# Kernel tuning notes

Measured on AMD Instinct MI355X. Metric: run time of the kernel, lower is better.

## Reference

```python
import jax, jax.numpy as jnp
import numpy as np

HEADS = 16
DIM_HEAD = 64
DIM = 1024
INNER = HEADS * DIM_HEAD


def setup_inputs() -> dict:
    key = jax.random.key(0)
    k1, k2, k3, k4 = jax.random.split(key, 4)
    x = jax.random.normal(k1, (4, 2048, DIM), dtype=jnp.float32)
    W_qkv = jax.random.normal(k2, (DIM, 3 * INNER), dtype=jnp.float32) * (DIM ** -0.5)
    W_out = jax.random.normal(k3, (INNER, DIM), dtype=jnp.float32) * (INNER ** -0.5)
    b_out = jax.random.normal(k4, (DIM,), dtype=jnp.float32) * 0.01
    temperature = jnp.asarray(np.log(DIM_HEAD ** -0.5), dtype=jnp.float32)
    return {"x": x, "W_qkv": W_qkv, "W_out": W_out, "b_out": b_out,
            "temperature": temperature}


def reference(x, W_qkv, W_out, b_out, temperature):
    b, n, _ = x.shape
    qkv = jnp.einsum('bnd,de->bne', x, W_qkv)  # [b, n, 3*inner]
    q, k, v = jnp.split(qkv, 3, axis=-1)
    def split_heads(t):
        return t.reshape(b, n, HEADS, DIM_HEAD).transpose(0, 2, 1, 3)  # b h n d
    q, k, v = split_heads(q), split_heads(k), split_heads(v)
    scale = jnp.exp(temperature)
    dots = jnp.einsum('bhid,bhjd->bhij', q, k) * scale  # [b, h, n, n]
    mask_value = -jnp.finfo(dots.dtype).max
    eye = jnp.eye(n, dtype=bool)
    dots = jnp.where(eye, mask_value, dots)
    attn = jax.nn.softmax(dots, axis=-1)
    out = jnp.einsum('bhij,bhjd->bhid', attn, v)  # [b, h, n, d]
    out = out.transpose(0, 2, 1, 3).reshape(b, n, INNER)
    return jnp.einsum('bni,id->bnd', out, W_out) + b_out
```

## Files before the change

### kernel.cpp

```cpp
#include <hip/hip_runtime.h>


using u16 = unsigned short;
typedef short short8 __attribute__((ext_vector_type(8)));
typedef float floatx4 __attribute__((ext_vector_type(4)));
typedef float floatx16 __attribute__((ext_vector_type(16)));
typedef unsigned int uint2v __attribute__((ext_vector_type(2)));

#define B_ 4
#define N_ 2048
#define H_ 16
#define DH_ 64
#define D_ 1024
#define INNER_ 1024
#define M_ (B_ * N_)

__device__ __forceinline__ float bf2f(u16 h) {
    union { unsigned u; float f; } c; c.u = ((unsigned)h) << 16; return c.f;
}
__device__ __forceinline__ u16 f2bf(float f) {
    union { float f; unsigned u; } c; c.f = f;
    unsigned u = c.u + 0x7fffu + ((c.u >> 16) & 1u);
    return (u16)(u >> 16);
}
__device__ __forceinline__ unsigned cvtpk_bf16(float lo, float hi) {
    unsigned r;
    asm("v_cvt_pk_bf16_f32 %0, %1, %2" : "=v"(r) : "v"(lo), "v"(hi));
    return r;
}
__device__ __forceinline__ float fast_exp2(float x) {
#if defined(__has_builtin) && __has_builtin(__builtin_amdgcn_exp2f)
    return __builtin_amdgcn_exp2f(x);
#else
    return __expf(x * 0.69314718056f);
#endif
}
__device__ __forceinline__ void gl2lds16(const u16* g, u16* l) {
    __builtin_amdgcn_global_load_lds(
        (const __attribute__((address_space(1))) void*)g,
        (__attribute__((address_space(3))) void*)l, 16, 0, 0);
}

__global__ void detect_prep(const u16* __restrict__ x, int* __restrict__ flag,
                            const void* __restrict__ bias_in,
                            const void* __restrict__ temp_in,
                            float* __restrict__ bias_f,
                            float* __restrict__ temp_f) {
    __shared__ int cnt;
    __shared__ int fl;
    if (threadIdx.x == 0) cnt = 0;
    __syncthreads();
    int c = 0;
    for (int i = threadIdx.x; i < 4096; i += 256) {
        int e = (x[i] >> 7) & 0xFF;
        if (e >= 107 && e <= 147) c++;
    }
    atomicAdd(&cnt, c);
    __syncthreads();
    if (threadIdx.x == 0) { fl = (cnt >= 3584) ? 1 : 0; flag[0] = fl; }
    __syncthreads();
    const int f = fl;
    for (int i = threadIdx.x; i < 1024; i += 256)
        bias_f[i] = f ? bf2f(((const u16*)bias_in)[i]) : ((const float*)bias_in)[i];
    if (threadIdx.x == 0)
        temp_f[0] = f ? bf2f(((const u16*)temp_in)[0]) : ((const float*)temp_in)[0];
}

__global__ __launch_bounds__(256) void prep_inputs(
    const void* __restrict__ x, u16* __restrict__ xb,
    const void* __restrict__ Wqkv, u16* __restrict__ Wqkv_t,
    const void* __restrict__ Wout, u16* __restrict__ Wout_t,
    const int* __restrict__ flag) {
    __shared__ u16 t[32][33];
    const int f = flag[0];
    const int b = blockIdx.x;
    if (b < 4096) {
        long i0 = ((long)b * 256 + threadIdx.x) * 8;
        u16 tmp[8];
        if (f) {
            *(short8*)tmp = *(const short8*)((const u16*)x + i0);
        } else {
            const float* p = (const float*)x + i0;
            for (int i = 0; i < 8; i++) tmp[i] = f2bf(p[i]);
        }
        *(short8*)&xb[i0] = *(const short8*)tmp;
        return;
    }
    const void* in;
    u16* out;
    int bx, by, R, C;
    if (b < 4096 + 3072) {
        int idx = b - 4096;
        bx = idx % 96; by = idx / 96; R = D_; C = 3 * INNER_;
        in = Wqkv; out = Wqkv_t;
    } else {
        int idx = b - 7168;
        bx = idx % 32; by = idx / 32; R = INNER_; C = D_;
        in = Wout; out = Wout_t;
    }
    int tx = threadIdx.x & 31, ty = threadIdx.x >> 5;
    int c0 = bx * 32, r0 = by * 32;
    for (int i = 0; i < 4; i++) {
        long idx = (long)(r0 + ty + i * 8) * C + c0 + tx;
        t[ty + i * 8][tx] = f ? ((const u16*)in)[idx] : f2bf(((const float*)in)[idx]);
    }
    __syncthreads();
    for (int i = 0; i < 4; i++)
        out[(long)(c0 + ty + i * 8) * R + r0 + tx] = t[tx][ty + i * 8];
}

__global__ __launch_bounds__(256) void transpose_v(
    const u16* __restrict__ in, u16* __restrict__ out) {
    __shared__ u16 t[32][33];
    const int bh = blockIdx.z;
    const u16* src = in + (long)bh * N_ * DH_;
    u16* dst = out + (long)bh * DH_ * N_;
    int tx = threadIdx.x & 31, ty = threadIdx.x >> 5;
    int r0 = blockIdx.y * 32;
    int c0 = blockIdx.x * 32;
    for (int i = 0; i < 4; i++)
        t[ty + i * 8][tx] = src[(long)(r0 + ty + i * 8) * DH_ + c0 + tx];
    __syncthreads();
    for (int i = 0; i < 4; i++)
        dst[(long)(c0 + ty + i * 8) * N_ + r0 + tx] = t[tx][ty + i * 8];
}

template <int MODE>
__global__ __launch_bounds__(256) void gemm_bt(
    const u16* __restrict__ A, const u16* __restrict__ Bt,
    int M, int N, int K,
    u16* __restrict__ out0, u16* __restrict__ out1, u16* __restrict__ out2,
    void* __restrict__ outv, const float* __restrict__ bias,
    const int* __restrict__ flag, const float* __restrict__ temp_f) {
    __shared__ __align__(16) u16 lA[128 * 32];
    __shared__ __align__(16) u16 lB[128 * 32];
    const int tid = threadIdx.x;
    const int lane = tid & 63;
    const int w = tid >> 6;
    const int wr = w >> 1, wc = w & 1;
    const int qd = lane >> 4, qm = lane & 15;
    const long m0 = (long)blockIdx.x * 128;
    const long n0 = (long)blockIdx.y * 128;

    floatx4 acc[4][4];
    for (int i = 0; i < 4; i++)
        for (int j = 0; j < 4; j++) acc[i][j] = (floatx4){0.f, 0.f, 0.f, 0.f};

    const int arow = lane >> 2;
    const int acol = ((lane & 3) ^ ((lane >> 3) & 3)) * 8;
    const int swz = (qm >> 1) & 3;

    for (int k0 = 0; k0 < K; k0 += 32) {
        for (int i = 0; i < 2; i++) {
            int c = w + i * 4;
            gl2lds16(A + (m0 + c * 16 + arow) * K + k0 + acol, lA + c * 512);
            gl2lds16(Bt + (n0 + c * 16 + arow) * K + k0 + acol, lB + c * 512);
        }
        __syncthreads();
        short8 af[4], bfr[4];
        for (int mt = 0; mt < 4; mt++)
            af[mt] = *(const short8*)&lA[(wr * 64 + mt * 16 + qm) * 32 + (qd ^ swz) * 8];
        for (int nt = 0; nt < 4; nt++)
            bfr[nt] = *(const short8*)&lB[(wc * 64 + nt * 16 + qm) * 32 + (qd ^ swz) * 8];
        for (int mt = 0; mt < 4; mt++)
            for (int nt = 0; nt < 4; nt++)
                acc[mt][nt] = __builtin_amdgcn_mfma_f32_16x16x32_bf16(
                    af[mt], bfr[nt], acc[mt][nt], 0, 0, 0);
        __syncthreads();
    }

    if (MODE == 0) {
        const float qscale = __expf(temp_f[0]) * 1.44269504089f;
        __shared__ __align__(16) u16 lC[64 * 132];
        for (int half = 0; half < 2; half++) {
            __syncthreads();
            if (wr == half) {
                for (int nt = 0; nt < 4; nt++) {
                    long ng = n0 + wc * 64 + nt * 16 + qm;
                    float sc = ((ng >> 10) == 0) ? qscale : 1.0f;
                    for (int mt = 0; mt < 4; mt++)
                        for (int r = 0; r < 4; r++)
                            lC[(mt * 16 + qd * 4 + r) * 132 + wc * 64 + nt * 16 + qm] =
                                f2bf(acc[mt][nt][r] * sc);
                }
            }
            __syncthreads();
            for (int i = 0; i < 4; i++) {
                int row = (tid >> 4) + i * 16;
                int c = (tid & 15) * 8;
                long m = m0 + half * 64 + row;
                long ngc = n0 + c;
                int part = (int)(ngc >> 10);
                int rem = (int)(ngc & 1023);
                int hh = rem >> 6, dh = rem & 63;
                long bb = m >> 11, n = m & 2047;
                long idx = ((bb * H_ + hh) * N_ + n) * DH_ + dh;
                short8 vv = *(const short8*)&lC[row * 132 + c];
                u16* dst = (part == 0) ? out0 : (part == 1) ? out1 : out2;
                *(short8*)&dst[idx] = vv;
            }
        }
    } else {
        const int f = flag[0];
        __shared__ __align__(16) float lCf[64 * 132];
        for (int half = 0; half < 2; half++) {
            __syncthreads();
            if (wr == half) {
                for (int nt = 0; nt < 4; nt++) {
                    long ng = n0 + wc * 64 + nt * 16 + qm;
                    float bv = bias[ng];
                    for (int mt = 0; mt < 4; mt++)
                        for (int r = 0; r < 4; r++)
                            lCf[(mt * 16 + qd * 4 + r) * 132 + wc * 64 + nt * 16 + qm] =
                                acc[mt][nt][r] + bv;
                }
            }
            __syncthreads();
            if (f) {
                for (int i = 0; i < 4; i++) {
                    int row = (tid >> 4) + i * 16;
                    int c = (tid & 15) * 8;
                    long m = m0 + half * 64 + row;
                    u16 tmp[8];
                    for (int j = 0; j < 8; j++) tmp[j] = f2bf(lCf[row * 132 + c + j]);
                    __builtin_nontemporal_store(*(const short8*)tmp,
                        (short8*)&((u16*)outv)[m * N + n0 + c]);
                }
            } else {
                for (int i = 0; i < 8; i++) {
                    int row = (tid >> 5) + i * 8;
                    int c = (tid & 31) * 4;
                    long m = m0 + half * 64 + row;
                    floatx4 vv = *(const floatx4*)&lCf[row * 132 + c];
                    __builtin_nontemporal_store(vv,
                        (floatx4*)&((float*)outv)[m * N + n0 + c]);
                }
            }
        }
    }
}

__global__ __launch_bounds__(256) void attn_full(
    const u16* __restrict__ q_ws, const u16* __restrict__ k_ws,
    const u16* __restrict__ vt_ws, u16* __restrict__ out) {
    __shared__ __align__(16) u16 lbuf[2 * 2 * 64 * 64];
    const int tid = threadIdx.x, lane = tid & 63, w = tid >> 6;
    const int ln = lane & 31, h = lane >> 5;

    int linear = blockIdx.y * 8 + blockIdx.x;
    int bh = (linear & 7) * 8 + ((linear >> 6) & 7);
    int q0 = ((linear >> 3) & 7) * 256;
    const int b = bh >> 4, hd = bh & 15;

    const u16* Q = q_ws + (long)bh * N_ * DH_;
    const u16* Kp = k_ws + (long)bh * N_ * DH_;
    const u16* Vt = vt_ws + (long)bh * DH_ * N_;

    const int qbase = q0 + w * 64;

    short8 qa[2][4];
#pragma unroll
    for (int g = 0; g < 2; g++)
#pragma unroll
        for (int c = 0; c < 4; c++)
            qa[g][c] = *(const short8*)
                &Q[(long)(qbase + g * 32 + ln) * DH_ + c * 16 + h * 8];

    floatx16 accO[2][2];
#pragma unroll
    for (int i = 0; i < 16; i++) {
        accO[0][0][i] = 0.f; accO[0][1][i] = 0.f;
        accO[1][0][i] = 0.f; accO[1][1][i] = 0.f;
    }
    float lacc[2] = {0.f, 0.f};

    const int srow = lane >> 3;
    const int scol = ((lane & 7) ^ srow) * 8;
    const int rsw = (ln & 7);

    {
        u16* nK = lbuf;
        u16* nV = lbuf + 4096;
        for (int i = 0; i < 2; i++) {
            int c = w + i * 4;
            gl2lds16(Kp + (long)(c * 8 + srow) * DH_ + scol, nK + c * 512);
            gl2lds16(Vt + (long)(c * 8 + srow) * N_ + scol, nV + c * 512);
        }
    }
    __syncthreads();

    for (int t = 0; t < 32; t++) {
        const int k0 = t * 64;
        const u16* lK = lbuf + (t & 1) * 8192;
        const u16* lV = lK + 4096;
        if (t < 31) {
            u16* nK = lbuf + ((t + 1) & 1) * 8192;
            u16* nV = nK + 4096;
            for (int i = 0; i < 2; i++) {
                int c = w + i * 4;
                gl2lds16(Kp + (long)(k0 + 64 + c * 8 + srow) * DH_ + scol,
                         nK + c * 512);
                gl2lds16(Vt + (long)(c * 8 + srow) * N_ + k0 + 64 + scol,
                         nV + c * 512);
            }
        }

#pragma unroll
        for (int kt = 0; kt < 2; kt++) {
            floatx16 accS[2];
#pragma unroll
            for (int i = 0; i < 16; i++) { accS[0][i] = 0.f; accS[1][i] = 0.f; }
#pragma unroll
            for (int c = 0; c < 4; c++) {
                short8 kf = *(const short8*)
                    &lK[(kt * 32 + ln) * 64 + ((c * 2 + h) ^ rsw) * 8];
                accS[0] = __builtin_amdgcn_mfma_f32_32x32x16_bf16(
                    kf, qa[0][c], accS[0], 0, 0, 0);
                accS[1] = __builtin_amdgcn_mfma_f32_32x32x16_bf16(
                    kf, qa[1][c], accS[1], 0, 0, 0);
            }
#pragma unroll
            for (int g = 0; g < 2; g++) {
#pragma unroll
                for (int r = 0; r < 16; r++)
                    accS[g][r] = fast_exp2(accS[g][r]);
                if ((qbase + g * 32) == (k0 + kt * 32)) {
#pragma unroll
                    for (int r = 0; r < 16; r++) {
                        int kk = (r & 3) + 8 * (r >> 2) + 4 * h;
                        if (kk == ln) accS[g][r] = 0.f;
                    }
                }
                float rs = (((accS[g][0] + accS[g][1]) + (accS[g][2] + accS[g][3]))
                          + ((accS[g][4] + accS[g][5]) + (accS[g][6] + accS[g][7])))
                         + (((accS[g][8] + accS[g][9]) + (accS[g][10] + accS[g][11]))
                          + ((accS[g][12] + accS[g][13]) + (accS[g][14] + accS[g][15])));
                lacc[g] += rs;
            }
#pragma unroll
            for (int ch = 0; ch < 2; ch++) {
                const int rb = ch * 8;
                short8 pfv[2];
#pragma unroll
                for (int g = 0; g < 2; g++) {
                    unsigned d01 = cvtpk_bf16(accS[g][rb + 0], accS[g][rb + 1]);
                    unsigned d23 = cvtpk_bf16(accS[g][rb + 2], accS[g][rb + 3]);
                    unsigned d45 = cvtpk_bf16(accS[g][rb + 4], accS[g][rb + 5]);
                    unsigned d67 = cvtpk_bf16(accS[g][rb + 6], accS[g][rb + 7]);
                    uint2v s1 = __builtin_amdgcn_permlane32_swap(d01, d45, false, false);
                    uint2v s2 = __builtin_amdgcn_permlane32_swap(d23, d67, false, false);
                    union { unsigned u[4]; short8 v; } pf;
                    pf.u[0] = s1[0]; pf.u[1] = s2[0]; pf.u[2] = s1[1]; pf.u[3] = s2[1];
                    pfv[g] = pf.v;
                }
                const int cc = kt * 2 + ch;
#pragma unroll
                for (int dt = 0; dt < 2; dt++) {
                    short8 vf = *(const short8*)
                        &lV[(dt * 32 + ln) * 64 + ((cc * 2 + h) ^ rsw) * 8];
                    accO[0][dt] = __builtin_amdgcn_mfma_f32_32x32x16_bf16(
                        vf, pfv[0], accO[0][dt], 0, 0, 0);
                    accO[1][dt] = __builtin_amdgcn_mfma_f32_32x32x16_bf16(
                        vf, pfv[1], accO[1][dt], 0, 0, 0);
                }
            }
        }
        __syncthreads();
    }

#pragma unroll
    for (int g = 0; g < 2; g++) {
        float s = lacc[g];
        s += __shfl_xor(s, 32, 64);
        const float inv = 1.f / s;
        u16* stg = (u16*)((char*)lbuf + w * 8192 + g * 4096);
#pragma unroll
        for (int dt = 0; dt < 2; dt++)
#pragma unroll
            for (int q2 = 0; q2 < 4; q2++) {
                union { unsigned u[2]; unsigned long long ull; } ee;
                ee.u[0] = cvtpk_bf16(accO[g][dt][q2 * 4 + 0] * inv,
                                     accO[g][dt][q2 * 4 + 1] * inv);
                ee.u[1] = cvtpk_bf16(accO[g][dt][q2 * 4 + 2] * inv,
                                     accO[g][dt][q2 * 4 + 3] * inv);
                int G = dt * 4 + q2;
                *(unsigned long long*)
                    &stg[ln * 64 + ((G ^ rsw) * 8) + h * 4] = ee.ull;
            }
    }
    __syncthreads();
#pragma unroll
    for (int p = 0; p < 8; p++) {
        int R = p * 32 + (tid >> 3);
        int G = tid & 7;
        const u16* src = (const u16*)((char*)lbuf + (R >> 6) * 8192
                          + ((R >> 5) & 1) * 4096
                          + (R & 31) * 128 + ((G ^ (R & 7)) * 16));
        short8 vv = *(const short8*)src;
        *(short8*)&out[((long)(b * N_ + q0 + R)) * INNER_ + hd * DH_ + G * 8] = vv;
    }
}

extern "C" void kernel_launch(void* const* d_in, const int* in_sizes, int n_in,
                              void* d_out, int out_size, void* d_ws, size_t ws_size,
                              hipStream_t stream) {
    const void* x    = d_in[0];
    const void* Wqkv = d_in[1];
    const void* Wout = d_in[2];
    const void* bout = d_in[3];
    const void* temp = d_in[4];

    char* base = (char*)d_ws;
    int*   flag    = (int*)base;
    float* temp_f  = (float*)(base + 16);
    float* bias_f  = (float*)(base + 32);
    u16* xb      = (u16*)(base + 8192);
    u16* Wqkv_t  = xb + (long)M_ * D_;
    u16* Wout_t  = Wqkv_t + 3072 * 1024;
    u16* q_ws    = Wout_t + 1024 * 1024;
    u16* k_ws    = q_ws + (long)B_ * H_ * N_ * DH_;
    u16* vt_ws   = k_ws + (long)B_ * H_ * N_ * DH_;
    u16* attn_out = vt_ws + (long)B_ * H_ * N_ * DH_;
    u16* v_nat   = attn_out;

    dim3 blk(256);
    detect_prep<<<1, blk, 0, stream>>>((const u16*)x, flag, bout, temp,
                                       bias_f, temp_f);
    prep_inputs<<<dim3(4096 + 3072 + 1024), blk, 0, stream>>>(
        x, xb, Wqkv, Wqkv_t, Wout, Wout_t, flag);
    gemm_bt<0><<<dim3(M_ / 128, 3 * INNER_ / 128), blk, 0, stream>>>(
        xb, Wqkv_t, M_, 3 * INNER_, D_, q_ws, k_ws, v_nat, nullptr, nullptr,
        flag, temp_f);
    transpose_v<<<dim3(DH_ / 32, N_ / 32, B_ * H_), blk, 0, stream>>>(
        v_nat, vt_ws);
    attn_full<<<dim3(8, 64), blk, 0, stream>>>(
        q_ws, k_ws, vt_ws, attn_out);
    gemm_bt<1><<<dim3(M_ / 128, D_ / 128), blk, 0, stream>>>(
        attn_out, Wout_t, M_, D_, INNER_, nullptr, nullptr, nullptr, d_out,
        bias_f, flag, temp_f);
}
```

Measured before the change: 285.7 us.

## Double-buffer GEMM LDS tiles and alias epilogue staging onto shared buffer

Turns the GEMM k-loop into a two-stage LDS double buffer. The next tile's global-to-LDS loads are issued before the MFMAs on the current tile, which removes one barrier per iteration and overlaps memory with compute. The epilogue staging buffers now reuse the same shared allocation, which keeps total LDS near its previous size. In MODE 1 the float staging pitch drops from 132 to 128 so it fits, at the risk of LDS bank conflicts in the epilogue writes.

```diff
diff --git a/kernel.cpp b/kernel.cpp
--- a/kernel.cpp
+++ b/kernel.cpp
@@ -132,8 +132,7 @@
     u16* __restrict__ out0, u16* __restrict__ out1, u16* __restrict__ out2,
     void* __restrict__ outv, const float* __restrict__ bias,
     const int* __restrict__ flag, const float* __restrict__ temp_f) {
-    __shared__ __align__(16) u16 lA[128 * 32];
-    __shared__ __align__(16) u16 lB[128 * 32];
+    __shared__ __align__(16) u16 smem[16384];
     const int tid = threadIdx.x;
     const int lane = tid & 63;
     const int w = tid >> 6;
@@ -150,13 +149,31 @@
     const int acol = ((lane & 3) ^ ((lane >> 3) & 3)) * 8;
     const int swz = (qm >> 1) & 3;
 
-    for (int k0 = 0; k0 < K; k0 += 32) {
+    {
+        u16* lA = smem;
+        u16* lB = smem + 4096;
         for (int i = 0; i < 2; i++) {
             int c = w + i * 4;
-            gl2lds16(A + (m0 + c * 16 + arow) * K + k0 + acol, lA + c * 512);
-            gl2lds16(Bt + (n0 + c * 16 + arow) * K + k0 + acol, lB + c * 512);
-        }
-        __syncthreads();
+            gl2lds16(A + (m0 + c * 16 + arow) * K + acol, lA + c * 512);
+            gl2lds16(Bt + (n0 + c * 16 + arow) * K + acol, lB + c * 512);
+        }
+    }
+    __syncthreads();
+
+    const int nT = K >> 5;
+    for (int t = 0; t < nT; ++t) {
+        const u16* lA = smem + (t & 1) * 8192;
+        const u16* lB = lA + 4096;
+        if (t + 1 < nT) {
+            u16* nA = smem + ((t + 1) & 1) * 8192;
+            u16* nB = nA + 4096;
+            const int k1 = (t + 1) << 5;
+            for (int i = 0; i < 2; i++) {
+                int c = w + i * 4;
+                gl2lds16(A + (m0 + c * 16 + arow) * K + k1 + acol, nA + c * 512);
+                gl2lds16(Bt + (n0 + c * 16 + arow) * K + k1 + acol, nB + c * 512);
+            }
+        }
         short8 af[4], bfr[4];
         for (int mt = 0; mt < 4; mt++)
             af[mt] = *(const short8*)&lA[(wr * 64 + mt * 16 + qm) * 32 + (qd ^ swz) * 8];
@@ -171,7 +188,7 @@
 
     if (MODE == 0) {
         const float qscale = __expf(temp_f[0]) * 1.44269504089f;
-        __shared__ __align__(16) u16 lC[64 * 132];
+        u16* lC = smem;
         for (int half = 0; half < 2; half++) {
             __syncthreads();
             if (wr == half) {
@@ -202,7 +219,7 @@
         }
     } else {
         const int f = flag[0];
-        __shared__ __align__(16) float lCf[64 * 132];
+        float* lCf = (float*)smem;
         for (int half = 0; half < 2; half++) {
             __syncthreads();
             if (wr == half) {
@@ -211,7 +228,7 @@
                     float bv = bias[ng];
                     for (int mt = 0; mt < 4; mt++)
                         for (int r = 0; r < 4; r++)
-                            lCf[(mt * 16 + qd * 4 + r) * 132 + wc * 64 + nt * 16 + qm] =
+                            lCf[(mt * 16 + qd * 4 + r) * 128 + wc * 64 + nt * 16 + qm] =
                                 acc[mt][nt][r] + bv;
                 }
             }
@@ -222,7 +239,7 @@
                     int c = (tid & 15) * 8;
                     long m = m0 + half * 64 + row;
                     u16 tmp[8];
-                    for (int j = 0; j < 8; j++) tmp[j] = f2bf(lCf[row * 132 + c + j]);
+                    for (int j = 0; j < 8; j++) tmp[j] = f2bf(lCf[row * 128 + c + j]);
                     __builtin_nontemporal_store(*(const short8*)tmp,
                         (short8*)&((u16*)outv)[m * N + n0 + c]);
                 }
@@ -231,7 +248,7 @@
                     int row = (tid >> 5) + i * 8;
                     int c = (tid & 31) * 4;
                     long m = m0 + half * 64 + row;
-                    floatx4 vv = *(const floatx4*)&lCf[row * 132 + c];
+                    floatx4 vv = *(const floatx4*)&lCf[row * 128 + c];
                     __builtin_nontemporal_store(vv,
                         (floatx4*)&((float*)outv)[m * N + n0 + c]);
                 }
```

Measured after the change: 289.4 us. About the same (+1.3%).

## Double-buffer GEMM LDS loads with larger 128x256 tiles and 512 threads

Applied to the files above, without the earlier changes.

The projection GEMM kernel moves to 512-thread blocks computing 128x256 output tiles with a K-step of 64. The next K-slice is prefetched into a second LDS buffer while the current one is consumed, which removes one barrier per iteration. The swizzle changes to an 8-way XOR and the epilogue reuses the shared buffer. The aim is to hide global-load latency and raise arithmetic intensity, at the cost of 96KB of LDS per block (lower occupancy) and fewer blocks in the grid.

```diff
diff --git a/kernel.cpp b/kernel.cpp
--- a/kernel.cpp
+++ b/kernel.cpp
@@ -126,112 +126,137 @@
 }
 
 template <int MODE>
-__global__ __launch_bounds__(256) void gemm_bt(
+__global__ __launch_bounds__(512) void gemm_bt(
     const u16* __restrict__ A, const u16* __restrict__ Bt,
     int M, int N, int K,
     u16* __restrict__ out0, u16* __restrict__ out1, u16* __restrict__ out2,
     void* __restrict__ outv, const float* __restrict__ bias,
     const int* __restrict__ flag, const float* __restrict__ temp_f) {
-    __shared__ __align__(16) u16 lA[128 * 32];
-    __shared__ __align__(16) u16 lB[128 * 32];
+    __shared__ __align__(16) u16 smem[49152];
     const int tid = threadIdx.x;
     const int lane = tid & 63;
     const int w = tid >> 6;
-    const int wr = w >> 1, wc = w & 1;
+    const int wm = w >> 2, wn = w & 3;
     const int qd = lane >> 4, qm = lane & 15;
     const long m0 = (long)blockIdx.x * 128;
-    const long n0 = (long)blockIdx.y * 128;
+    const long n0 = (long)blockIdx.y * 256;
 
     floatx4 acc[4][4];
     for (int i = 0; i < 4; i++)
         for (int j = 0; j < 4; j++) acc[i][j] = (floatx4){0.f, 0.f, 0.f, 0.f};
 
-    const int arow = lane >> 2;
-    const int acol = ((lane & 3) ^ ((lane >> 3) & 3)) * 8;
-    const int swz = (qm >> 1) & 3;
-
-    for (int k0 = 0; k0 < K; k0 += 32) {
-        for (int i = 0; i < 2; i++) {
-            int c = w + i * 4;
-            gl2lds16(A + (m0 + c * 16 + arow) * K + k0 + acol, lA + c * 512);
-            gl2lds16(Bt + (n0 + c * 16 + arow) * K + k0 + acol, lB + c * 512);
-        }
-        __syncthreads();
-        short8 af[4], bfr[4];
-        for (int mt = 0; mt < 4; mt++)
-            af[mt] = *(const short8*)&lA[(wr * 64 + mt * 16 + qm) * 32 + (qd ^ swz) * 8];
-        for (int nt = 0; nt < 4; nt++)
-            bfr[nt] = *(const short8*)&lB[(wc * 64 + nt * 16 + qm) * 32 + (qd ^ swz) * 8];
-        for (int mt = 0; mt < 4; mt++)
-            for (int nt = 0; nt < 4; nt++)
-                acc[mt][nt] = __builtin_amdgcn_mfma_f32_16x16x32_bf16(
-                    af[mt], bfr[nt], acc[mt][nt], 0, 0, 0);
+    const int sr = tid >> 3;
+    const int sg = tid & 7;
+    const int scol = (sg ^ (sr & 7)) * 8;
+    const int rx = qm & 7;
+
+    for (int c = 0; c < 2; c++)
+        gl2lds16(A + (m0 + c * 64 + sr) * K + scol, smem + c * 4096 + tid * 8);
+    for (int c = 0; c < 4; c++)
+        gl2lds16(Bt + (n0 + c * 64 + sr) * K + scol,
+                 smem + 8192 + c * 4096 + tid * 8);
+    __syncthreads();
+
+    const int nT = K >> 6;
+    for (int t = 0; t < nT; ++t) {
+        const u16* lA = smem + (t & 1) * 24576;
+        const u16* lB = lA + 8192;
+        if (t + 1 < nT) {
+            u16* nb = smem + ((t + 1) & 1) * 24576;
+            const int k1 = (t + 1) << 6;
+            for (int c = 0; c < 2; c++)
+                gl2lds16(A + (m0 + c * 64 + sr) * K + k1 + scol,
+                         nb + c * 4096 + tid * 8);
+            for (int c = 0; c < 4; c++)
+                gl2lds16(Bt + (n0 + c * 64 + sr) * K + k1 + scol,
+                         nb + 8192 + c * 4096 + tid * 8);
+        }
+#pragma unroll
+        for (int s = 0; s < 2; s++) {
+            short8 af[4], bf[4];
+#pragma unroll
+            for (int mr = 0; mr < 4; mr++)
+                af[mr] = *(const short8*)
+                    &lA[(wm * 64 + mr * 16 + qm) * 64 + (((s * 4 + qd) ^ rx) * 8)];
+#pragma unroll
+            for (int nr = 0; nr < 4; nr++)
+                bf[nr] = *(const short8*)
+                    &lB[(wn * 64 + nr * 16 + qm) * 64 + (((s * 4 + qd) ^ rx) * 8)];
+#pragma unroll
+            for (int mr = 0; mr < 4; mr++)
+#pragma unroll
+                for (int nr = 0; nr < 4; nr++)
+                    acc[mr][nr] = __builtin_amdgcn_mfma_f32_16x16x32_bf16(
+                        af[mr], bf[nr], acc[mr][nr], 0, 0, 0);
+        }
         __syncthreads();
     }
 
     if (MODE == 0) {
         const float qscale = __expf(temp_f[0]) * 1.44269504089f;
-        __shared__ __align__(16) u16 lC[64 * 132];
+        const int part = (int)(n0 >> 10);
+        const float sc = (part == 0) ? qscale : 1.0f;
+        u16* lC = smem;
         for (int half = 0; half < 2; half++) {
             __syncthreads();
-            if (wr == half) {
-                for (int nt = 0; nt < 4; nt++) {
-                    long ng = n0 + wc * 64 + nt * 16 + qm;
-                    float sc = ((ng >> 10) == 0) ? qscale : 1.0f;
-                    for (int mt = 0; mt < 4; mt++)
+            if (wm == half) {
+                for (int nr = 0; nr < 4; nr++) {
+                    int col = wn * 64 + nr * 16 + qm;
+                    for (int mr = 0; mr < 4; mr++)
                         for (int r = 0; r < 4; r++)
-                            lC[(mt * 16 + qd * 4 + r) * 132 + wc * 64 + nt * 16 + qm] =
-                                f2bf(acc[mt][nt][r] * sc);
+                            lC[(mr * 16 + qd * 4 + r) * 264 + col] =
+                                f2bf(acc[mr][nr][r] * sc);
                 }
             }
             __syncthreads();
+            const long mb = m0 + half * 64;
+            const long bb = mb >> 11;
+            const int  nb = (int)(mb & 2047);
             for (int i = 0; i < 4; i++) {
-                int row = (tid >> 4) + i * 16;
-                int c = (tid & 15) * 8;
-                long m = m0 + half * 64 + row;
+                int row = (tid >> 5) + i * 16;
+                int c = (tid & 31) * 8;
                 long ngc = n0 + c;
-                int part = (int)(ngc >> 10);
+                int pt = (int)(ngc >> 10);
                 int rem = (int)(ngc & 1023);
                 int hh = rem >> 6, dh = rem & 63;
-                long bb = m >> 11, n = m & 2047;
-                long idx = ((bb * H_ + hh) * N_ + n) * DH_ + dh;
-                short8 vv = *(const short8*)&lC[row * 132 + c];
-                u16* dst = (part == 0) ? out0 : (part == 1) ? out1 : out2;
+                long idx = ((bb * H_ + hh) * N_ + (nb + row)) * DH_ + dh;
+                short8 vv = *(const short8*)&lC[row * 264 + c];
+                u16* dst = (pt == 0) ? out0 : (pt == 1) ? out1 : out2;
                 *(short8*)&dst[idx] = vv;
             }
         }
     } else {
         const int f = flag[0];
-        __shared__ __align__(16) float lCf[64 * 132];
+        float* lCf = (float*)smem;
         for (int half = 0; half < 2; half++) {
             __syncthreads();
-            if (wr == half) {
-                for (int nt = 0; nt < 4; nt++) {
-                    long ng = n0 + wc * 64 + nt * 16 + qm;
+            if (wm == half) {
+                for (int nr = 0; nr < 4; nr++) {
+                    long ng = n0 + wn * 64 + nr * 16 + qm;
                     float bv = bias[ng];
-                    for (int mt = 0; mt < 4; mt++)
+                    for (int mr = 0; mr < 4; mr++)
                         for (int r = 0; r < 4; r++)
-                            lCf[(mt * 16 + qd * 4 + r) * 132 + wc * 64 + nt * 16 + qm] =
-                                acc[mt][nt][r] + bv;
+                            lCf[(mr * 16 + qd * 4 + r) * 260 + wn * 64 + nr * 16 + qm] =
+                                acc[mr][nr][r] + bv;
                 }
             }
             __syncthreads();
             if (f) {
                 for (int i = 0; i < 4; i++) {
-                    int row = (tid >> 4) + i * 16;
-                    int c = (tid & 15) * 8;
+                    int row = (tid >> 5) + i * 16;
+                    int c = (tid & 31) * 8;
                     long m = m0 + half * 64 + row;
                     u16 tmp[8];
-                    for (int j = 0; j < 8; j++) tmp[j] = f2bf(lCf[row * 132 + c + j]);
+                    for (int j = 0; j < 8; j++) tmp[j] = f2bf(lCf[row * 260 + c + j]);
                     __builtin_nontemporal_store(*(const short8*)tmp,
                         (short8*)&((u16*)outv)[m * N + n0 + c]);
                 }
             } else {
                 for (int i = 0; i < 8; i++) {
-                    int row = (tid >> 5) + i * 8;
-                    int c = (tid & 31) * 4;
+                    int row = (tid >> 6) + i * 8;
+                    int c = (tid & 63) * 4;
                     long m = m0 + half * 64 + row;
-                    floatx4 vv = *(const floatx4*)&lCf[row * 132 + c];
+                    floatx4 vv = *(const floatx4*)&lCf[row * 260 + c];
                     __builtin_nontemporal_store(vv,
                         (floatx4*)&((float*)outv)[m * N + n0 + c]);
                 }
@@ -428,14 +453,14 @@
                                        bias_f, temp_f);
     prep_inputs<<<dim3(4096 + 3072 + 1024), blk, 0, stream>>>(
         x, xb, Wqkv, Wqkv_t, Wout, Wout_t, flag);
-    gemm_bt<0><<<dim3(M_ / 128, 3 * INNER_ / 128), blk, 0, stream>>>(
+    gemm_bt<0><<<dim3(M_ / 128, 3 * INNER_ / 256), dim3(512), 0, stream>>>(
         xb, Wqkv_t, M_, 3 * INNER_, D_, q_ws, k_ws, v_nat, nullptr, nullptr,
         flag, temp_f);
     transpose_v<<<dim3(DH_ / 32, N_ / 32, B_ * H_), blk, 0, stream>>>(
         v_nat, vt_ws);
     attn_full<<<dim3(8, 64), blk, 0, stream>>>(
         q_ws, k_ws, vt_ws, attn_out);
-    gemm_bt<1><<<dim3(M_ / 128, D_ / 128), blk, 0, stream>>>(
+    gemm_bt<1><<<dim3(M_ / 128, D_ / 256), dim3(512), 0, stream>>>(
         attn_out, Wout_t, M_, D_, INNER_, nullptr, nullptr, nullptr, d_out,
         bias_f, flag, temp_f);
 }
```

New measurement: 276.7 us. 3.1% less time.
